# Kernel optimization log

Hardware: AMD Instinct MI355X
Metric: run time of the kernel (lower is better)

The kernel has to match this reference:

```python
import jax, jax.numpy as jnp
import numpy as np

N = 8192
IN_F = 512
OUT_F = 64
ALPHA = 0.2        # LeakyReLU slope
L_ITERS = 3        # RobustSum iterations
EPS = 0.01
GAMMA = 4.0
T = 1.0
NEG_BIG = -9e15


def setup_inputs() -> dict:
    key = jax.random.key(0)
    k1, k2, k3, k4 = jax.random.split(key, 4)
    x = jax.random.normal(k1, (N, IN_F), dtype=jnp.float32)
    adj = jax.random.randint(k2, (N, N), 0, 2, dtype=jnp.int32)
    # xavier-uniform-like init scales
    limW = 1.414 * np.sqrt(6.0 / (IN_F + OUT_F))
    W = jax.random.uniform(k3, (IN_F, OUT_F), dtype=jnp.float32, minval=-limW, maxval=limW)
    lima = 1.414 * np.sqrt(6.0 / (2 * OUT_F + 1))
    a = jax.random.uniform(k4, (2 * OUT_F, 1), dtype=jnp.float32, minval=-lima, maxval=lima)
    return {"adj": adj, "input": x, "W": W, "a": a}


def _robust_sum_mcp(A, V):
    # M = A @ V, then IRLS-style reweighted aggregation (norm='MCP')
    M = A @ V
    for _ in range(L_ITERS):
        Md = jax.lax.stop_gradient(M)
        Vd = jax.lax.stop_gradient(V)
        # pairwise Euclidean distance [N, N] (fused form of torch.cdist)
        d2 = (jnp.sum(Md * Md, axis=1, keepdims=True)
              + jnp.sum(Vd * Vd, axis=1)[None, :]
              - 2.0 * (Md @ Vd.T))
        dist = jnp.sqrt(jnp.maximum(d2, 0.0))
        w = 1.0 / (dist + EPS) - 1.0 / GAMMA
        w = jnp.maximum(w, EPS)          # w[w < eps] = eps
        ww = w * A
        denom = jnp.maximum(jnp.sum(jnp.abs(ww), axis=-1, keepdims=True), 1e-12)
        ww_norm = ww / denom             # F.normalize(p=1, dim=-1)
        M = (1.0 - T) * M + T * (ww_norm @ V)
    return M


def reference(adj, input, W, a):
    adj_f = adj.astype(jnp.float32)
    h = input @ W                                     # [N, OUT_F]
    a1 = a[:OUT_F, 0]                                 # [OUT_F]
    a2 = a[OUT_F:, 0]                                 # [OUT_F]
    # fused equivalent of cat([h_i, h_j]) @ a : e_ij = lrelu(h_i.a1 + h_j.a2)
    e = jax.nn.leaky_relu((h @ a1)[:, None] + (h @ a2)[None, :], ALPHA)  # [N, N]
    scores = adj_f * e + (1.0 - adj_f) * NEG_BIG
    attention = jax.nn.softmax(scores, axis=1)
    # dropout omitted (eval mode / dropout=0.0)
    h_prime = _robust_sum_mcp(attention, h)
    return jax.nn.elu(h_prime)                        # concat=True
```

## Files before the change

### kernel.cpp

```cpp
#include <hip/hip_runtime.h>
#include <hip/hip_bf16.h>

typedef __attribute__((ext_vector_type(8))) short s8v;
typedef __attribute__((ext_vector_type(4))) short s4v;
typedef __attribute__((ext_vector_type(4))) float f4v;

static __device__ __forceinline__ short f2bf(float f){
  unsigned int u = __float_as_uint(f);
  u = (u + 0x7FFFu + ((u >> 16) & 1u)) >> 16;
  return (short)u;
}

static __device__ __forceinline__ s4v pack4(float a, float b, float c, float d){
  union { s4v v; __hip_bfloat162 h[2]; } u;
  u.h[0] = __float22bfloat162_rn(make_float2(a, b));
  u.h[1] = __float22bfloat162_rn(make_float2(c, d));
  return u.v;
}

static __device__ __forceinline__ f4v mfma16(s4v a, s4v b, f4v c){
  return __builtin_amdgcn_mfma_f32_16x16x16bf16_1k(a, b, c, 0, 0, 0);
}

__global__ __launch_bounds__(256) void k_h(const float* __restrict__ x,
                                           const float* __restrict__ W,
                                           float* __restrict__ h){
  int wid = threadIdx.x >> 6, lane = threadIdx.x & 63;
  int r0 = (blockIdx.x * 4 + wid) * 8;
  const float* xr = x + (size_t)r0 * 512;
  float acc[8] = {0.f,0.f,0.f,0.f,0.f,0.f,0.f,0.f};
  #pragma unroll 4
  for (int k = 0; k < 512; ++k){
    float wv = W[k*64 + lane];
    #pragma unroll
    for (int r = 0; r < 8; ++r)
      acc[r] = fmaf(xr[(size_t)r*512 + k], wv, acc[r]);
  }
  #pragma unroll
  for (int r = 0; r < 8; ++r)
    h[(size_t)(r0 + r)*64 + lane] = acc[r];
}

__global__ __launch_bounds__(256) void k_prep(const float* __restrict__ h,
                                              const float* __restrict__ a,
                                              short* __restrict__ VbfSw,
                                              short* __restrict__ VTsw,
                                              float* __restrict__ F,
                                              float2* __restrict__ EG,
                                              float* __restrict__ V2arr,
                                              float* __restrict__ Pv2,
                                              float* __restrict__ Pg,
                                              float* __restrict__ Vpart){
  __shared__ float t[64][65];
  const int tid = threadIdx.x;
  const int lane = tid & 63, w = tid >> 6;
  const int lo = lane & 15, hi = lane >> 4;
  const int i0 = blockIdx.x * 64;
  #pragma unroll
  for (int it = 0; it < 16; ++it){
    int r = w * 16 + it;
    t[r][lane] = h[(size_t)(i0 + r) * 64 + lane];
  }
  __syncthreads();
  #pragma unroll
  for (int ks = 0; ks < 2; ++ks){
    s8v o;
    #pragma unroll
    for (int e = 0; e < 8; ++e)
      o[e] = f2bf(t[w*16 + lo][ks*32 + hi*8 + e]);
    *(s8v*)(VbfSw + ((size_t)(i0/16 + w)*2 + ks)*512 + lane*8) = o;
  }
  const int p = w >> 1;
  #pragma unroll
  for (int oo = 0; oo < 2; ++oo){
    const int ot = (w & 1) * 2 + oo;
    s8v o;
    #pragma unroll
    for (int e = 0; e < 8; ++e){
      int parity = e >> 2, q = e & 3;
      o[e] = f2bf(t[(p*2 + parity)*16 + hi*4 + q][ot*16 + lo]);
    }
    *(s8v*)(VTsw + ((size_t)(i0/32 + p)*4 + ot)*512 + lane*8) = o;
  }
  if (tid < 64){
    const int r = tid;
    float f = 0.f, g = 0.f, v2 = 0.f;
    #pragma unroll 8
    for (int o = 0; o < 64; ++o){
      float hv = t[r][o];
      f  = fmaf(hv, a[o],      f);
      g  = fmaf(hv, a[64 + o], g);
      v2 = fmaf(hv, hv,        v2);
    }
    const int row = i0 + r;
    F[row] = f;
    V2arr[row] = v2;
    EG[row] = make_float2(__expf(g), __expf(0.2f * g));
    float vmin = v2, gmx = g;
    #pragma unroll
    for (int off = 32; off; off >>= 1){
      vmin = fminf(vmin, __shfl_xor(vmin, off));
      gmx  = fmaxf(gmx,  __shfl_xor(gmx,  off));
    }
    if (r == 0){ Pv2[blockIdx.x] = vmin; Pg[blockIdx.x] = gmx; }
    float cs = 0.f;
    #pragma unroll 8
    for (int rr = 0; rr < 64; ++rr) cs += t[rr][tid];
    Vpart[(size_t)blockIdx.x * 64 + tid] = cs;
  }
}

__global__ __launch_bounds__(512, 4) void k_fused(
    const int* __restrict__ adj,
    const float2* __restrict__ EG, const float* __restrict__ V2arr,
    const float* __restrict__ F,
    const float* __restrict__ Pv2, const float* __restrict__ Pg,
    const float* __restrict__ Vpart,
    const short* __restrict__ VbfSw, const short* __restrict__ VTsw,
    unsigned long long* __restrict__ adjbits,
    float* __restrict__ out)
{
  __shared__ float numT[8][64][16];
  __shared__ float denL[8][16];
  __shared__ float Mlds[16][68];
  __shared__ float M1L[16][68];
  __shared__ __align__(16) short Mb16[16][64];
  __shared__ float CiL[16], rm2L[16], uaiL[16];
  __shared__ float VmeanL[64];
  __shared__ float gmaxS, v2minS;
  __shared__ int actL, chgL, emptyL;

  const int tid  = threadIdx.x;
  const int w    = tid >> 6;
  const int lane = tid & 63;
  const int lo = lane & 15, hi = lane >> 4;
  const int r0 = blockIdx.x << 4;
  const int i  = r0 + lo;

  if (tid < 64){
    float v = fminf(Pv2[tid], Pv2[tid + 64]);
    float g = fmaxf(Pg[tid],  Pg[tid + 64]);
    #pragma unroll
    for (int off = 32; off; off >>= 1){
      v = fminf(v, __shfl_xor(v, off));
      g = fmaxf(g, __shfl_xor(g, off));
    }
    if (tid == 0){ v2minS = v; gmaxS = g; actL = 0; emptyL = 0; }
  }
  __syncthreads();

  const float fi   = F[i];
  const float gmax = gmaxS;
  const float z    = fi + gmax;
  const float B    = fmaxf(z, 0.2f * z);
  const float e1s  = __expf(fi - B);
  const float e2s  = __expf(0.2f * fi - B);

  const int* arow = adj + (size_t)i * 8192 + hi*4;

  const f4v zero4 = {0.f,0.f,0.f,0.f};
  f4v pacc[4] = {zero4, zero4, zero4, zero4};
  float pden = 0.f;

  for (int c = w; c < 128; c += 8){
    const int* ap = arow + (c << 6);
    s4v wwpk[4];
    unsigned long long mrow = 0ull;
    #pragma unroll
    for (int nt = 0; nt < 4; ++nt){
      const int jb = (c << 6) + nt*16 + hi*4;
      const int4 av4 = *(const int4*)(ap + nt*16);
      const int ab[4] = {av4.x, av4.y, av4.z, av4.w};
      const f4v u0 = *(const f4v*)(EG + jb);
      const f4v u1 = *(const f4v*)(EG + jb + 2);
      const float ega[4] = {u0[0], u0[2], u1[0], u1[2]};
      const float egb[4] = {u0[1], u0[3], u1[1], u1[3]};
      float wwv[4];
      #pragma unroll
      for (int q = 0; q < 4; ++q){
        float u = fmaxf(e1s * ega[q], e2s * egb[q]);
        u = ab[q] ? u : 0.f;
        pden += u;
        wwv[q] = u;
      }
      const unsigned nib = (unsigned)ab[0] | ((unsigned)ab[1] << 1)
                         | ((unsigned)ab[2] << 2) | ((unsigned)ab[3] << 3);
      mrow |= (unsigned long long)nib << (nt*16 + hi*4);
      wwpk[nt] = pack4(wwv[0], wwv[1], wwv[2], wwv[3]);
    }
    mrow |= __shfl_xor(mrow, 16);
    mrow |= __shfl_xor(mrow, 32);
    if (hi == 0) adjbits[(size_t)c * 8192 + i] = mrow;

    const short* vt = VTsw + (size_t)c*4096 + lane*8;
    #pragma unroll
    for (int p = 0; p < 2; ++p){
      #pragma unroll
      for (int ot = 0; ot < 4; ++ot){
        s8v v8 = *(const s8v*)(vt + (p*4 + ot)*512);
        s4v aLo = {v8[0], v8[1], v8[2], v8[3]};
        s4v aHi = {v8[4], v8[5], v8[6], v8[7]};
        pacc[ot] = mfma16(aLo, wwpk[2*p],   pacc[ot]);
        pacc[ot] = mfma16(aHi, wwpk[2*p+1], pacc[ot]);
      }
    }
  }

  pden += __shfl_xor(pden, 16);
  pden += __shfl_xor(pden, 32);
  if (lane < 16) denL[w][lane] = pden;
  #pragma unroll
  for (int ot = 0; ot < 4; ++ot)
    #pragma unroll
    for (int q = 0; q < 4; ++q)
      numT[w][ot*16 + hi*4 + q][lo] = pacc[ot][q];
  __syncthreads();

  {
    const int ii = tid & 15;
    const int o  = tid >> 4;
    float den = 0.f;
    #pragma unroll
    for (int w2 = 0; w2 < 8; ++w2) den += denL[w2][ii];
    if (o == 0){
      uaiL[ii] = (den <= 0.f) ? (1.0f / 8192.0f) : 0.f;
      if (den <= 0.f) emptyL = 1;
    }
    den = fmaxf(den, 1e-30f);
    const float rden = 1.0f / den;
    #pragma unroll
    for (int rep = 0; rep < 2; ++rep){
      const int oo = o + rep*32;
      float num = 0.f;
      #pragma unroll
      for (int w2 = 0; w2 < 8; ++w2) num += numT[w2][oo][ii];
      Mlds[ii][oo] = num * rden;
    }
    if (tid < 16){
      float fb = F[r0 + tid];
      float zb = fb + gmax;
      float Bb = fmaxf(zb, 0.2f * zb);
      CiL[tid] = Bb + __logf(den);
    }
  }
  __syncthreads();

  if (emptyL){
    if (tid < 64){
      float s = 0.f;
      for (int b = 0; b < 128; ++b) s += Vpart[(size_t)b*64 + tid];
      VmeanL[tid] = s * (1.0f / 8192.0f);
    }
    __syncthreads();
    {
      const int r = tid >> 5, c2 = (tid & 31) << 1;
      if (uaiL[r] > 0.f){ Mlds[r][c2] = VmeanL[c2]; Mlds[r][c2+1] = VmeanL[c2+1]; }
    }
    __syncthreads();
  }

  if (tid < 16){
    float s2 = 0.f;
    #pragma unroll 8
    for (int o = 0; o < 64; ++o) s2 = fmaf(Mlds[tid][o], Mlds[tid][o], s2);
    rm2L[tid] = s2;
    if (sqrtf(s2) > sqrtf(v2minS) - 3.85f) actL = 1;
  }
  __syncthreads();

  if (actL){
    {
      const int r = tid >> 5, c2 = (tid & 31) << 1;
      float a0 = Mlds[r][c2], a1 = Mlds[r][c2+1];
      M1L[r][c2] = a0;  M1L[r][c2+1] = a1;
      Mb16[r][c2] = f2bf(a0); Mb16[r][c2+1] = f2bf(a1);
    }
    const float e1c = __expf(fi - CiL[lo]);
    const float e2c = __expf(0.2f * fi - CiL[lo]);
    const float uai = uaiL[lo];
    __syncthreads();

    for (int pass = 0; pass < 3; ++pass){
      if (tid == 0) chgL = 0;
      __syncthreads();
      const float rm2 = rm2L[lo];
      s8v bM[2];
      #pragma unroll
      for (int ks = 0; ks < 2; ++ks)
        bM[ks] = *(const s8v*)&Mb16[lo][ks*32 + hi*8];

      f4v cacc[4] = {zero4, zero4, zero4, zero4};
      float cden = 0.f;

      for (int c = w; c < 128; c += 8){
        f4v acc[4] = {zero4, zero4, zero4, zero4};
        const short* vb = VbfSw + (size_t)c*4096 + lane*8;
        #pragma unroll
        for (int nt = 0; nt < 4; ++nt){
          #pragma unroll
          for (int ks = 0; ks < 2; ++ks){
            s8v av = *(const s8v*)(vb + (nt*2 + ks)*512);
            acc[nt] = __builtin_amdgcn_mfma_f32_16x16x32_bf16(av, bM[ks], acc[nt], 0, 0, 0);
          }
        }
        f4v d2s[4];
        float dmin = 1e30f;
        #pragma unroll
        for (int nt = 0; nt < 4; ++nt){
          const int jb = (c << 6) + nt*16 + hi*4;
          const f4v v2q = *(const f4v*)(V2arr + jb);
          #pragma unroll
          for (int q = 0; q < 4; ++q){
            float d2 = fmaf(-2.0f, acc[nt][q], rm2 + v2q[q]);
            d2s[nt][q] = d2;
            dmin = fminf(dmin, d2);
          }
        }
        if (__any(dmin < 14.75f)){
          const unsigned long long mrow = adjbits[(size_t)c * 8192 + i];
          s4v wwpk[4];
          #pragma unroll
          for (int nt = 0; nt < 4; ++nt){
            const int jb = (c << 6) + nt*16 + hi*4;
            const unsigned nib = (unsigned)(mrow >> (nt*16 + hi*4)) & 0xFu;
            const f4v u0 = *(const f4v*)(EG + jb);
            const f4v u1 = *(const f4v*)(EG + jb + 2);
            const float ega[4] = {u0[0], u0[2], u1[0], u1[2]};
            const float egb[4] = {u0[1], u0[3], u1[1], u1[3]};
            float wwv[4];
            #pragma unroll
            for (int q = 0; q < 4; ++q){
              float A = fmaxf(e1c * ega[q], e2c * egb[q]);
              A = ((nib >> q) & 1u) ? A : uai;
              float dist  = sqrtf(fmaxf(d2s[nt][q], 0.f));
              float delta = fmaxf(__builtin_amdgcn_rcpf(dist + 0.01f) - 0.26f, 0.f);
              float ww = delta * A;
              cden += ww;
              wwv[q] = ww;
            }
            wwpk[nt] = pack4(wwv[0], wwv[1], wwv[2], wwv[3]);
          }
          const short* vt = VTsw + (size_t)c*4096 + lane*8;
          #pragma unroll
          for (int p = 0; p < 2; ++p){
            #pragma unroll
            for (int ot = 0; ot < 4; ++ot){
              s8v v8 = *(const s8v*)(vt + (p*4 + ot)*512);
              s4v aLo = {v8[0], v8[1], v8[2], v8[3]};
              s4v aHi = {v8[4], v8[5], v8[6], v8[7]};
              cacc[ot] = mfma16(aLo, wwpk[2*p],   cacc[ot]);
              cacc[ot] = mfma16(aHi, wwpk[2*p+1], cacc[ot]);
            }
          }
        }
      }

      if (__any(cden > 0.f)) chgL = 1;
      __syncthreads();
      if (!chgL) break;
      {
        float cd = cden;
        cd += __shfl_xor(cd, 16);
        cd += __shfl_xor(cd, 32);
        if (lane < 16) denL[w][lane] = cd;
        #pragma unroll
        for (int ot = 0; ot < 4; ++ot)
          #pragma unroll
          for (int q = 0; q < 4; ++q)
            numT[w][ot*16 + hi*4 + q][lo] = cacc[ot][q];
        __syncthreads();
        {
          const int ii = tid & 15;
          const int o  = tid >> 4;
          float den = 0.f;
          #pragma unroll
          for (int w2 = 0; w2 < 8; ++w2) den += denL[w2][ii];
          const float rden = 1.0f / (0.01f + den);
          #pragma unroll
          for (int rep = 0; rep < 2; ++rep){
            const int oo = o + rep*32;
            float num = 0.f;
            #pragma unroll
            for (int w2 = 0; w2 < 8; ++w2) num += numT[w2][oo][ii];
            Mlds[ii][oo] = fmaf(0.01f, M1L[ii][oo], num) * rden;
          }
        }
        __syncthreads();
        {
          const int r = tid >> 5, c2 = (tid & 31) << 1;
          Mb16[r][c2]   = f2bf(Mlds[r][c2]);
          Mb16[r][c2+1] = f2bf(Mlds[r][c2+1]);
        }
        if (tid < 16){
          float s2 = 0.f;
          #pragma unroll 8
          for (int o = 0; o < 64; ++o) s2 = fmaf(Mlds[tid][o], Mlds[tid][o], s2);
          rm2L[tid] = s2;
        }
        __syncthreads();
      }
    }
  }
  __syncthreads();

  #pragma unroll
  for (int rr = 0; rr < 2; ++rr){
    const int ir = w*2 + rr;
    const float v = Mlds[ir][lane];
    out[(size_t)(r0 + ir) * 64 + lane] = (v > 0.f) ? v : (__expf(v) - 1.0f);
  }
}

extern "C" void kernel_launch(void* const* d_in, const int* in_sizes, int n_in,
                              void* d_out, int out_size, void* d_ws, size_t ws_size,
                              hipStream_t stream){
  (void)in_sizes; (void)n_in; (void)out_size; (void)ws_size;
  const int*   adj = (const int*)d_in[0];
  const float* x   = (const float*)d_in[1];
  const float* W   = (const float*)d_in[2];
  const float* a   = (const float*)d_in[3];
  float* out = (float*)d_out;
  char* ws = (char*)d_ws;

  float* h     = (float*)(ws);
  short* VbfSw = (short*)(ws + (2u << 20));
  short* VTsw  = (short*)(ws + (3u << 20));
  float* F     = (float*)(ws + (4u << 20));
  float* V2arr = (float*)(ws + (4u << 20) + (32u << 10));
  float2* EG   = (float2*)(ws + (4u << 20) + (64u << 10));
  float* Vpart = (float*)(ws + (4u << 20) + (128u << 10));
  float* Pv2   = (float*)(ws + (4u << 20) + (160u << 10));
  float* Pg    = (float*)(ws + (4u << 20) + (161u << 10));
  unsigned long long* adjbits = (unsigned long long*)(ws + (5u << 20));

  k_h    <<<256, 256, 0, stream>>>(x, W, h);
  k_prep <<<128, 256, 0, stream>>>(h, a, VbfSw, VTsw, F, EG, V2arr, Pv2, Pg, Vpart);
  k_fused<<<512, 512, 0, stream>>>(adj, EG, V2arr, F, Pv2, Pg, Vpart, VbfSw, VTsw, adjbits, out);
}
```

Baseline: 142.3 us.

## Split fused kernel into per-pass kernels with column-halved blocks

Breaks the single fused attention+IRLS kernel into separate kernels: an attention/first-aggregation kernel, a middle normalisation kernel, three per-pass reweighting kernels and a final ELU kernel. Each row group is now split across two blocks covering column halves, doubling the grid to 1024 blocks and raising the occupancy hint, with partial numerators and denominators written to global memory and combined by the next kernel. This targets low parallelism and occupancy from 512 blocks each doing long serial passes, at the cost of extra launches, global round-trips of partial sums and the loss of the early-exit convergence break.

Measured after the change: 337.8 us. +137.3%, slower.

```diff
diff --git a/kernel.cpp b/kernel.cpp
--- a/kernel.cpp
+++ b/kernel.cpp
@@ -110,59 +110,49 @@
   }
 }
 
-__global__ __launch_bounds__(512, 4) void k_fused(
+__global__ __launch_bounds__(512, 6) void k_ab(
     const int* __restrict__ adj,
-    const float2* __restrict__ EG, const float* __restrict__ V2arr,
-    const float* __restrict__ F,
-    const float* __restrict__ Pv2, const float* __restrict__ Pg,
-    const float* __restrict__ Vpart,
-    const short* __restrict__ VbfSw, const short* __restrict__ VTsw,
+    const float2* __restrict__ EG, const float* __restrict__ F,
+    const float* __restrict__ Pg,
+    const short* __restrict__ VTsw,
     unsigned long long* __restrict__ adjbits,
-    float* __restrict__ out)
+    float* __restrict__ pnum, float* __restrict__ pden)
 {
   __shared__ float numT[8][64][16];
   __shared__ float denL[8][16];
-  __shared__ float Mlds[16][68];
-  __shared__ float M1L[16][68];
-  __shared__ __align__(16) short Mb16[16][64];
-  __shared__ float CiL[16], rm2L[16], uaiL[16];
-  __shared__ float VmeanL[64];
-  __shared__ float gmaxS, v2minS;
-  __shared__ int actL, chgL, emptyL;
+  __shared__ float gmaxS;
 
   const int tid  = threadIdx.x;
   const int w    = tid >> 6;
   const int lane = tid & 63;
   const int lo = lane & 15, hi = lane >> 4;
-  const int r0 = blockIdx.x << 4;
+  const int b  = blockIdx.x;
+  const int g  = b >> 1, chalf = b & 1;
+  const int r0 = g << 4;
   const int i  = r0 + lo;
 
   if (tid < 64){
-    float v = fminf(Pv2[tid], Pv2[tid + 64]);
-    float g = fmaxf(Pg[tid],  Pg[tid + 64]);
-    #pragma unroll
-    for (int off = 32; off; off >>= 1){
-      v = fminf(v, __shfl_xor(v, off));
-      g = fmaxf(g, __shfl_xor(g, off));
-    }
-    if (tid == 0){ v2minS = v; gmaxS = g; actL = 0; emptyL = 0; }
-  }
-  __syncthreads();
-
-  const float fi   = F[i];
-  const float gmax = gmaxS;
-  const float z    = fi + gmax;
-  const float B    = fmaxf(z, 0.2f * z);
-  const float e1s  = __expf(fi - B);
-  const float e2s  = __expf(0.2f * fi - B);
+    float gm = fmaxf(Pg[tid], Pg[tid + 64]);
+    #pragma unroll
+    for (int off = 32; off; off >>= 1) gm = fmaxf(gm, __shfl_xor(gm, off));
+    if (tid == 0) gmaxS = gm;
+  }
+  __syncthreads();
+
+  const float fi = F[i];
+  const float z  = fi + gmaxS;
+  const float B  = fmaxf(z, 0.2f * z);
+  const float e1s = __expf(fi - B);
+  const float e2s = __expf(0.2f * fi - B);
 
   const int* arow = adj + (size_t)i * 8192 + hi*4;
-
   const f4v zero4 = {0.f,0.f,0.f,0.f};
   f4v pacc[4] = {zero4, zero4, zero4, zero4};
-  float pden = 0.f;
-
-  for (int c = w; c < 128; c += 8){
+  float pd = 0.f;
+
+  const int cbase = chalf << 6;
+  for (int k = 0; k < 8; ++k){
+    const int c = cbase + w + (k << 3);
     const int* ap = arow + (c << 6);
     s4v wwpk[4];
     unsigned long long mrow = 0ull;
@@ -180,7 +170,7 @@
       for (int q = 0; q < 4; ++q){
         float u = fmaxf(e1s * ega[q], e2s * egb[q]);
         u = ab[q] ? u : 0.f;
-        pden += u;
+        pd += u;
         wwv[q] = u;
       }
       const unsigned nib = (unsigned)ab[0] | ((unsigned)ab[1] << 1)
@@ -206,9 +196,9 @@
     }
   }
 
-  pden += __shfl_xor(pden, 16);
-  pden += __shfl_xor(pden, 32);
-  if (lane < 16) denL[w][lane] = pden;
+  pd += __shfl_xor(pd, 16);
+  pd += __shfl_xor(pd, 32);
+  if (lane < 16) denL[w][lane] = pd;
   #pragma unroll
   for (int ot = 0; ot < 4; ++ot)
     #pragma unroll
@@ -222,193 +212,261 @@
     float den = 0.f;
     #pragma unroll
     for (int w2 = 0; w2 < 8; ++w2) den += denL[w2][ii];
-    if (o == 0){
-      uaiL[ii] = (den <= 0.f) ? (1.0f / 8192.0f) : 0.f;
-      if (den <= 0.f) emptyL = 1;
-    }
-    den = fmaxf(den, 1e-30f);
-    const float rden = 1.0f / den;
+    if (o == 0) pden[b*16 + ii] = den;
     #pragma unroll
     for (int rep = 0; rep < 2; ++rep){
       const int oo = o + rep*32;
       float num = 0.f;
       #pragma unroll
       for (int w2 = 0; w2 < 8; ++w2) num += numT[w2][oo][ii];
-      Mlds[ii][oo] = num * rden;
-    }
-    if (tid < 16){
-      float fb = F[r0 + tid];
-      float zb = fb + gmax;
-      float Bb = fmaxf(zb, 0.2f * zb);
-      CiL[tid] = Bb + __logf(den);
-    }
-  }
-  __syncthreads();
-
-  if (emptyL){
+      pnum[((size_t)b*16 + ii)*64 + oo] = num;
+    }
+  }
+}
+
+__global__ __launch_bounds__(256) void k_mid(
+    const float* __restrict__ F,
+    const float* __restrict__ Pg,
+    const float* __restrict__ Vpart,
+    const float* __restrict__ pnum, const float* __restrict__ pden,
+    float* __restrict__ M1G, float* __restrict__ CiG, float* __restrict__ uaiG)
+{
+  __shared__ float gmaxS;
+  __shared__ float VmeanL[64];
+  __shared__ int emptyB;
+
+  const int tid = threadIdx.x;
+  if (tid == 0) emptyB = 0;
+  if (tid < 64){
+    float gm = fmaxf(Pg[tid], Pg[tid + 64]);
+    #pragma unroll
+    for (int off = 32; off; off >>= 1) gm = fmaxf(gm, __shfl_xor(gm, off));
+    if (tid == 0) gmaxS = gm;
+  }
+  __syncthreads();
+
+  const int r  = blockIdx.x * 64 + (tid >> 2);
+  const int cs = (tid & 3) << 4;
+  const int g  = r >> 4, ri = r & 15;
+  const float den = pden[(2*g)*16 + ri] + pden[(2*g+1)*16 + ri];
+
+  if ((tid & 3) == 0){
+    uaiG[r] = (den <= 0.f) ? (1.0f / 8192.0f) : 0.f;
+    const float z = F[r] + gmaxS;
+    const float Bb = fmaxf(z, 0.2f * z);
+    CiG[r] = Bb + __logf(fmaxf(den, 1e-30f));
+    if (den <= 0.f) emptyB = 1;
+  }
+  __syncthreads();
+  if (emptyB){
     if (tid < 64){
       float s = 0.f;
-      for (int b = 0; b < 128; ++b) s += Vpart[(size_t)b*64 + tid];
+      for (int bb = 0; bb < 128; ++bb) s += Vpart[(size_t)bb*64 + tid];
       VmeanL[tid] = s * (1.0f / 8192.0f);
     }
     __syncthreads();
-    {
-      const int r = tid >> 5, c2 = (tid & 31) << 1;
-      if (uaiL[r] > 0.f){ Mlds[r][c2] = VmeanL[c2]; Mlds[r][c2+1] = VmeanL[c2+1]; }
-    }
-    __syncthreads();
-  }
-
+  }
+
+  const float rden = 1.0f / fmaxf(den, 1e-30f);
+  const size_t p0 = ((size_t)(2*g)*16 + ri)*64;
+  const size_t p1 = ((size_t)(2*g+1)*16 + ri)*64;
+  #pragma unroll 4
+  for (int o = cs; o < cs + 16; ++o){
+    float m = (pnum[p0 + o] + pnum[p1 + o]) * rden;
+    if (den <= 0.f) m = VmeanL[o];
+    M1G[(size_t)r*64 + o] = m;
+  }
+}
+
+__global__ __launch_bounds__(512, 6) void k_pass(
+    const int pass,
+    const float2* __restrict__ EG, const float* __restrict__ V2arr,
+    const float* __restrict__ F,
+    const float* __restrict__ Pv2,
+    const short* __restrict__ VbfSw, const short* __restrict__ VTsw,
+    const unsigned long long* __restrict__ adjbits,
+    const float* __restrict__ M1G, const float* __restrict__ CiG,
+    const float* __restrict__ uaiG,
+    const float* __restrict__ cnum_in, const float* __restrict__ cden_in,
+    float* __restrict__ cnum_out, float* __restrict__ cden_out)
+{
+  __shared__ float numT[8][64][16];
+  __shared__ float denL[8][16];
+  __shared__ __align__(16) short Mb16[16][64];
+  __shared__ float rm2L[16];
+  __shared__ float v2minS;
+  __shared__ int actL;
+
+  const int tid  = threadIdx.x;
+  const int w    = tid >> 6;
+  const int lane = tid & 63;
+  const int lo = lane & 15, hi = lane >> 4;
+  const int b  = blockIdx.x;
+  const int g  = b >> 1, chalf = b & 1;
+  const int r0 = g << 4;
+  const int i  = r0 + lo;
+
+  if (tid < 64){
+    float v = fminf(Pv2[tid], Pv2[tid + 64]);
+    #pragma unroll
+    for (int off = 32; off; off >>= 1) v = fminf(v, __shfl_xor(v, off));
+    if (tid == 0){ v2minS = v; actL = 0; }
+  }
+
+  {
+    const int ri = tid >> 5;
+    const int cc = (tid & 31) << 1;
+    const size_t rbase = (size_t)(r0 + ri)*64;
+    float m0 = M1G[rbase + cc];
+    float m1 = M1G[rbase + cc + 1];
+    if (pass > 1){
+      const float cdp = cden_in[(2*g)*16 + ri] + cden_in[(2*g+1)*16 + ri];
+      if (cdp > 0.f){
+        const size_t p0 = ((size_t)(2*g)*16 + ri)*64;
+        const size_t p1 = ((size_t)(2*g+1)*16 + ri)*64;
+        const float rd = 1.0f / (0.01f + cdp);
+        m0 = fmaf(0.01f, m0, cnum_in[p0 + cc]     + cnum_in[p1 + cc])     * rd;
+        m1 = fmaf(0.01f, m1, cnum_in[p0 + cc + 1] + cnum_in[p1 + cc + 1]) * rd;
+      }
+    }
+    Mb16[ri][cc]     = f2bf(m0);
+    Mb16[ri][cc + 1] = f2bf(m1);
+    float s2 = fmaf(m0, m0, m1*m1);
+    #pragma unroll
+    for (int off = 1; off < 32; off <<= 1) s2 += __shfl_xor(s2, off);
+    if ((lane & 31) == 0) rm2L[ri] = s2;
+  }
+  __syncthreads();
   if (tid < 16){
-    float s2 = 0.f;
-    #pragma unroll 8
-    for (int o = 0; o < 64; ++o) s2 = fmaf(Mlds[tid][o], Mlds[tid][o], s2);
-    rm2L[tid] = s2;
-    if (sqrtf(s2) > sqrtf(v2minS) - 3.85f) actL = 1;
+    if (sqrtf(rm2L[tid]) > sqrtf(v2minS) - 3.85f) actL = 1;
   }
   __syncthreads();
 
   if (actL){
-    {
-      const int r = tid >> 5, c2 = (tid & 31) << 1;
-      float a0 = Mlds[r][c2], a1 = Mlds[r][c2+1];
-      M1L[r][c2] = a0;  M1L[r][c2+1] = a1;
-      Mb16[r][c2] = f2bf(a0); Mb16[r][c2+1] = f2bf(a1);
-    }
-    const float e1c = __expf(fi - CiL[lo]);
-    const float e2c = __expf(0.2f * fi - CiL[lo]);
-    const float uai = uaiL[lo];
-    __syncthreads();
-
-    for (int pass = 0; pass < 3; ++pass){
-      if (tid == 0) chgL = 0;
-      __syncthreads();
-      const float rm2 = rm2L[lo];
-      s8v bM[2];
-      #pragma unroll
-      for (int ks = 0; ks < 2; ++ks)
-        bM[ks] = *(const s8v*)&Mb16[lo][ks*32 + hi*8];
-
-      f4v cacc[4] = {zero4, zero4, zero4, zero4};
-      float cden = 0.f;
-
-      for (int c = w; c < 128; c += 8){
-        f4v acc[4] = {zero4, zero4, zero4, zero4};
-        const short* vb = VbfSw + (size_t)c*4096 + lane*8;
+    const float fi  = F[i];
+    const float e1c = __expf(fi - CiG[i]);
+    const float e2c = __expf(0.2f * fi - CiG[i]);
+    const float uai = uaiG[i];
+    const float rm2 = rm2L[lo];
+    const f4v zero4 = {0.f,0.f,0.f,0.f};
+    s8v bM[2];
+    #pragma unroll
+    for (int ks = 0; ks < 2; ++ks)
+      bM[ks] = *(const s8v*)&Mb16[lo][ks*32 + hi*8];
+
+    f4v cacc[4] = {zero4, zero4, zero4, zero4};
+    float cden = 0.f;
+
+    const int cbase = chalf << 6;
+    for (int k = 0; k < 8; ++k){
+      const int c = cbase + w + (k << 3);
+      f4v acc[4] = {zero4, zero4, zero4, zero4};
+      const short* vb = VbfSw + (size_t)c*4096 + lane*8;
+      #pragma unroll
+      for (int nt = 0; nt < 4; ++nt){
         #pragma unroll
-        for (int nt = 0; nt < 4; ++nt){
-          #pragma unroll
-          for (int ks = 0; ks < 2; ++ks){
-            s8v av = *(const s8v*)(vb + (nt*2 + ks)*512);
-            acc[nt] = __builtin_amdgcn_mfma_f32_16x16x32_bf16(av, bM[ks], acc[nt], 0, 0, 0);
-          }
+        for (int ks = 0; ks < 2; ++ks){
+          s8v av = *(const s8v*)(vb + (nt*2 + ks)*512);
+          acc[nt] = __builtin_amdgcn_mfma_f32_16x16x32_bf16(av, bM[ks], acc[nt], 0, 0, 0);
         }
-        f4v d2s[4];
-        float dmin = 1e30f;
+      }
+      float dmin = 1e30f;
+      #pragma unroll
+      for (int nt = 0; nt < 4; ++nt){
+        const int jb = (c << 6) + nt*16 + hi*4;
+        const f4v v2q = *(const f4v*)(V2arr + jb);
+        #pragma unroll
+        for (int q = 0; q < 4; ++q){
+          const float d2 = fmaf(-2.0f, acc[nt][q], rm2 + v2q[q]);
+          acc[nt][q] = d2;
+          dmin = fminf(dmin, d2);
+        }
+      }
+      if (__any(dmin < 14.75f)){
+        const unsigned long long mrow = adjbits[(size_t)c * 8192 + i];
+        s4v wwpk[4];
         #pragma unroll
         for (int nt = 0; nt < 4; ++nt){
           const int jb = (c << 6) + nt*16 + hi*4;
-          const f4v v2q = *(const f4v*)(V2arr + jb);
+          const unsigned nib = (unsigned)(mrow >> (nt*16 + hi*4)) & 0xFu;
+          const f4v u0 = *(const f4v*)(EG + jb);
+          const f4v u1 = *(const f4v*)(EG + jb + 2);
+          const float ega[4] = {u0[0], u0[2], u1[0], u1[2]};
+          const float egb[4] = {u0[1], u0[3], u1[1], u1[3]};
+          float wwv[4];
           #pragma unroll
           for (int q = 0; q < 4; ++q){
-            float d2 = fmaf(-2.0f, acc[nt][q], rm2 + v2q[q]);
-            d2s[nt][q] = d2;
-            dmin = fminf(dmin, d2);
+            float A = fmaxf(e1c * ega[q], e2c * egb[q]);
+            A = ((nib >> q) & 1u) ? A : uai;
+            const float dist  = sqrtf(fmaxf(acc[nt][q], 0.f));
+            const float delta = fmaxf(__builtin_amdgcn_rcpf(dist + 0.01f) - 0.26f, 0.f);
+            const float ww = delta * A;
+            cden += ww;
+            wwv[q] = ww;
+          }
+          wwpk[nt] = pack4(wwv[0], wwv[1], wwv[2], wwv[3]);
+        }
+        const short* vt = VTsw + (size_t)c*4096 + lane*8;
+        #pragma unroll
+        for (int p = 0; p < 2; ++p){
+          #pragma unroll
+          for (int ot = 0; ot < 4; ++ot){
+            s8v v8 = *(const s8v*)(vt + (p*4 + ot)*512);
+            s4v aLo = {v8[0], v8[1], v8[2], v8[3]};
+            s4v aHi = {v8[4], v8[5], v8[6], v8[7]};
+            cacc[ot] = mfma16(aLo, wwpk[2*p],   cacc[ot]);
+            cacc[ot] = mfma16(aHi, wwpk[2*p+1], cacc[ot]);
           }
         }
-        if (__any(dmin < 14.75f)){
-          const unsigned long long mrow = adjbits[(size_t)c * 8192 + i];
-          s4v wwpk[4];
-          #pragma unroll
-          for (int nt = 0; nt < 4; ++nt){
-            const int jb = (c << 6) + nt*16 + hi*4;
-            const unsigned nib = (unsigned)(mrow >> (nt*16 + hi*4)) & 0xFu;
-            const f4v u0 = *(const f4v*)(EG + jb);
-            const f4v u1 = *(const f4v*)(EG + jb + 2);
-            const float ega[4] = {u0[0], u0[2], u1[0], u1[2]};
-            const float egb[4] = {u0[1], u0[3], u1[1], u1[3]};
-            float wwv[4];
-            #pragma unroll
-            for (int q = 0; q < 4; ++q){
-              float A = fmaxf(e1c * ega[q], e2c * egb[q]);
-              A = ((nib >> q) & 1u) ? A : uai;
-              float dist  = sqrtf(fmaxf(d2s[nt][q], 0.f));
-              float delta = fmaxf(__builtin_amdgcn_rcpf(dist + 0.01f) - 0.26f, 0.f);
-              float ww = delta * A;
-              cden += ww;
-              wwv[q] = ww;
-            }
-            wwpk[nt] = pack4(wwv[0], wwv[1], wwv[2], wwv[3]);
-          }
-          const short* vt = VTsw + (size_t)c*4096 + lane*8;
-          #pragma unroll
-          for (int p = 0; p < 2; ++p){
-            #pragma unroll
-            for (int ot = 0; ot < 4; ++ot){
-              s8v v8 = *(const s8v*)(vt + (p*4 + ot)*512);
-              s4v aLo = {v8[0], v8[1], v8[2], v8[3]};
-              s4v aHi = {v8[4], v8[5], v8[6], v8[7]};
-              cacc[ot] = mfma16(aLo, wwpk[2*p],   cacc[ot]);
-              cacc[ot] = mfma16(aHi, wwpk[2*p+1], cacc[ot]);
-            }
-          }
-        }
-      }
-
-      if (__any(cden > 0.f)) chgL = 1;
-      __syncthreads();
-      if (!chgL) break;
-      {
-        float cd = cden;
-        cd += __shfl_xor(cd, 16);
-        cd += __shfl_xor(cd, 32);
-        if (lane < 16) denL[w][lane] = cd;
+      }
+    }
+
+    cden += __shfl_xor(cden, 16);
+    cden += __shfl_xor(cden, 32);
+    if (lane < 16) denL[w][lane] = cden;
+    #pragma unroll
+    for (int ot = 0; ot < 4; ++ot)
+      #pragma unroll
+      for (int q = 0; q < 4; ++q)
+        numT[w][ot*16 + hi*4 + q][lo] = cacc[ot][q];
+    __syncthreads();
+    {
+      const int ii = tid & 15;
+      const int o  = tid >> 4;
+      float den = 0.f;
+      #pragma unroll
+      for (int w2 = 0; w2 < 8; ++w2) den += denL[w2][ii];
+      if (o == 0) cden_out[b*16 + ii] = den;
+      #pragma unroll
+      for (int rep = 0; rep < 2; ++rep){
+        const int oo = o + rep*32;
+        float num = 0.f;
         #pragma unroll
-        for (int ot = 0; ot < 4; ++ot)
-          #pragma unroll
-          for (int q = 0; q < 4; ++q)
-            numT[w][ot*16 + hi*4 + q][lo] = cacc[ot][q];
-        __syncthreads();
-        {
-          const int ii = tid & 15;
-          const int o  = tid >> 4;
-          float den = 0.f;
-          #pragma unroll
-          for (int w2 = 0; w2 < 8; ++w2) den += denL[w2][ii];
-          const float rden = 1.0f / (0.01f + den);
-          #pragma unroll
-          for (int rep = 0; rep < 2; ++rep){
-            const int oo = o + rep*32;
-            float num = 0.f;
-            #pragma unroll
-            for (int w2 = 0; w2 < 8; ++w2) num += numT[w2][oo][ii];
-            Mlds[ii][oo] = fmaf(0.01f, M1L[ii][oo], num) * rden;
-          }
-        }
-        __syncthreads();
-        {
-          const int r = tid >> 5, c2 = (tid & 31) << 1;
-          Mb16[r][c2]   = f2bf(Mlds[r][c2]);
-          Mb16[r][c2+1] = f2bf(Mlds[r][c2+1]);
-        }
-        if (tid < 16){
-          float s2 = 0.f;
-          #pragma unroll 8
-          for (int o = 0; o < 64; ++o) s2 = fmaf(Mlds[tid][o], Mlds[tid][o], s2);
-          rm2L[tid] = s2;
-        }
-        __syncthreads();
-      }
-    }
-  }
-  __syncthreads();
-
-  #pragma unroll
-  for (int rr = 0; rr < 2; ++rr){
-    const int ir = w*2 + rr;
-    const float v = Mlds[ir][lane];
-    out[(size_t)(r0 + ir) * 64 + lane] = (v > 0.f) ? v : (__expf(v) - 1.0f);
-  }
+        for (int w2 = 0; w2 < 8; ++w2) num += numT[w2][oo][ii];
+        cnum_out[((size_t)b*16 + ii)*64 + oo] = num;
+      }
+    }
+  } else {
+    if (tid < 16) cden_out[b*16 + tid] = 0.f;
+  }
+}
+
+__global__ __launch_bounds__(256) void k_fin(
+    const float* __restrict__ M1G,
+    const float* __restrict__ cnum_in, const float* __restrict__ cden_in,
+    float* __restrict__ out)
+{
+  const int idx = blockIdx.x * 256 + threadIdx.x;
+  const int r = idx >> 6, o = idx & 63;
+  const int g = r >> 4, ri = r & 15;
+  const float cdp = cden_in[(2*g)*16 + ri] + cden_in[(2*g+1)*16 + ri];
+  float m = M1G[(size_t)r*64 + o];
+  if (cdp > 0.f){
+    const float n = cnum_in[((size_t)(2*g)*16 + ri)*64 + o]
+                  + cnum_in[((size_t)(2*g+1)*16 + ri)*64 + o];
+    m = fmaf(0.01f, m, n) / (0.01f + cdp);
+  }
+  out[idx] = (m > 0.f) ? m : (__expf(m) - 1.0f);
 }
 
 extern "C" void kernel_launch(void* const* d_in, const int* in_sizes, int n_in,
@@ -423,6 +481,7 @@
   char* ws = (char*)d_ws;
 
   float* h     = (float*)(ws);
+  float* M1G   = (float*)(ws);
   short* VbfSw = (short*)(ws + (2u << 20));
   short* VTsw  = (short*)(ws + (3u << 20));
   float* F     = (float*)(ws + (4u << 20));
@@ -431,9 +490,25 @@
   float* Vpart = (float*)(ws + (4u << 20) + (128u << 10));
   float* Pv2   = (float*)(ws + (4u << 20) + (160u << 10));
   float* Pg    = (float*)(ws + (4u << 20) + (161u << 10));
-  unsigned long long* adjbits = (unsigned long long*)(ws + (5u << 20));
+  float* CiG   = (float*)(ws + (4u << 20) + (192u << 10));
+  float* uaiG  = (float*)(ws + (4u << 20) + (224u << 10));
+  float* pnum  = (float*)(ws + (5u << 20));
+  float* pden  = (float*)(ws + (9u << 20));
+  float* cnumA = (float*)(ws + (10u << 20));
+  float* cdenA = (float*)(ws + (14u << 20));
+  float* cnumB = (float*)(ws + (15u << 20));
+  float* cdenB = (float*)(ws + (19u << 20));
+  unsigned long long* adjbits = (unsigned long long*)(ws + (20u << 20));
 
   k_h    <<<256, 256, 0, stream>>>(x, W, h);
   k_prep <<<128, 256, 0, stream>>>(h, a, VbfSw, VTsw, F, EG, V2arr, Pv2, Pg, Vpart);
-  k_fused<<<512, 512, 0, stream>>>(adj, EG, V2arr, F, Pv2, Pg, Vpart, VbfSw, VTsw, adjbits, out);
-}
+  k_ab   <<<1024, 512, 0, stream>>>(adj, EG, F, Pg, VTsw, adjbits, pnum, pden);
+  k_mid  <<<128, 256, 0, stream>>>(F, Pg, Vpart, pnum, pden, M1G, CiG, uaiG);
+  k_pass <<<1024, 512, 0, stream>>>(1, EG, V2arr, F, Pv2, VbfSw, VTsw, adjbits,
+                                    M1G, CiG, uaiG, cnumB, cdenB, cnumA, cdenA);
+  k_pass <<<1024, 512, 0, stream>>>(2, EG, V2arr, F, Pv2, VbfSw, VTsw, adjbits,
+                                    M1G, CiG, uaiG, cnumA, cdenA, cnumB, cdenB);
+  k_pass <<<1024, 512, 0, stream>>>(3, EG, V2arr, F, Pv2, VbfSw, VTsw, adjbits,
+                                    M1G, CiG, uaiG, cnumB, cdenB, cnumA, cdenA);
+  k_fin  <<<2048, 256, 0, stream>>>(M1G, cnumA, cdenA, out);
+}
```
